# Optimization experiments

Hardware: AMD Instinct MI355X
Metric: run time of the kernel (lower is better)

Reference implementation:

```python
import jax, jax.numpy as jnp
import numpy as np

K = 1024   # codebook size
C = 8      # codebook channels
D = K // C # per-channel code dim = 128
BETA = 0.25
B = 8192   # batch of latent vectors, each of size C*D = K


def setup_inputs() -> dict:
    key = jax.random.key(0)
    k1, k2, k3 = jax.random.split(key, 3)
    latents = jax.random.normal(k1, (B, C * D), dtype=jnp.float32)
    # nn.Embedding(K, D) init: uniform(-1/K, 1/K)
    embedding = jax.random.uniform(k2, (K, D), dtype=jnp.float32,
                                   minval=-1.0 / K, maxval=1.0 / K)
    k = jax.random.randint(k3, (C,), 0, 8, dtype=jnp.int32)
    return {"latents": latents, "embedding": embedding, "k": k}


def reference(latents, embedding, k):
    sg = jax.lax.stop_gradient
    flat = latents.reshape(-1, D)                                  # [B*C, D]
    # squared euclidean distance to every code: [B*C, K]
    dist = (jnp.sum(flat ** 2, axis=1, keepdims=True)
            + jnp.sum(embedding ** 2, axis=1)
            - 2.0 * (flat @ embedding.T))
    order = jnp.argsort(dist, axis=1).reshape(-1, C, K)            # [B, C, K]
    # per channel c, pick the k[c]-th nearest code index
    sel = jnp.take_along_axis(order, k[None, :, None], axis=2)[..., 0]  # [B, C]
    # one-hot @ embedding == plain gather of selected rows
    quantized = embedding[sel.reshape(-1)].reshape(latents.shape)  # [B, C*D]
    commitment_loss = jnp.mean((sg(quantized) - latents) ** 2)
    embedding_loss = jnp.mean((quantized - sg(latents)) ** 2)
    vq_loss = BETA * commitment_loss + embedding_loss
    # straight-through estimator
    quantized_st = latents + sg(quantized - latents)
    return quantized_st, vq_loss
```

## Files before the change

### kernel.cpp

```cpp
#include <hip/hip_runtime.h>

#define KDIM   128
#define BM     64
#define NELEM  8388608

#define OFF_EBUF0 17408
#define OFF_ESQ   33792
#define OFF_FSQ   37888
#define OFF_SEL   38144
#define SMEM_SZ   38400

typedef __attribute__((ext_vector_type(8)))  short  short8;
typedef __attribute__((ext_vector_type(8)))  __bf16 bf16x8;
typedef __attribute__((ext_vector_type(4)))  float  f32x4;

__device__ inline ushort f2bf(float f) {
  unsigned u = __builtin_bit_cast(unsigned, f);
  u += 0x7fffu + ((u >> 16) & 1u);
  return (ushort)(u >> 16);
}
__device__ inline f32x4 mfma16(short8 a, short8 b, f32x4 c) {
  return __builtin_amdgcn_mfma_f32_16x16x32_bf16(
      __builtin_bit_cast(bf16x8, a), __builtin_bit_cast(bf16x8, b), c, 0, 0, 0);
}
__device__ inline void gload16(const void* g, void* l) {
  __builtin_amdgcn_global_load_lds(
      (const __attribute__((address_space(1))) unsigned*)g,
      (__attribute__((address_space(3))) unsigned*)l, 16, 0, 0);
}

__global__ void vq_prep(const float* __restrict__ emb, ushort* __restrict__ ebf,
                        float* __restrict__ esqm) {
  int j = blockIdx.x, d = threadIdx.x;
  float v = emb[j * KDIM + d];
  ebf[j * KDIM + (d ^ ((j & 7) << 3))] = f2bf(v);
  float s = v * v;
#pragma unroll
  for (int m = 1; m <= 32; m <<= 1) s += __shfl_xor(s, m);
  __shared__ float w[2];
  if ((threadIdx.x & 63) == 0) w[threadIdx.x >> 6] = s;
  __syncthreads();
  if (threadIdx.x == 0) esqm[j] = -0.5f * (w[0] + w[1]);
}

__global__ __launch_bounds__(256, 4) void vq_main(
    const float* __restrict__ lat, const float* __restrict__ emb,
    const int* __restrict__ ksel, const ushort* __restrict__ ebf,
    const float* __restrict__ esqm, float* __restrict__ out,
    float* __restrict__ partial) {
  __shared__ __align__(16) unsigned char smem[SMEM_SZ];
  ushort* fLds    = (ushort*)(smem);
  float*  esqmLds = (float*)(smem + OFF_ESQ);
  float*  fsqLds  = (float*)(smem + OFF_FSQ);
  int*    selLds  = (int*)(smem + OFF_SEL);

  const int tid = threadIdx.x;
  const int lane = tid & 63, wid = tid >> 6;
  const int gR0 = blockIdx.x * BM;

  {
    const char* src = (const char*)ebf + tid * 16;
    char* dst = (char*)smem + OFF_EBUF0 + tid * 16;
#pragma unroll
    for (int q = 0; q < 4; ++q) gload16(src + q * 4096, dst + q * 4096);
  }
  ((float4*)esqmLds)[tid] = ((const float4*)esqm)[tid];

#pragma unroll
  for (int it = 0; it < 8; ++it) {
    int i = tid + it * 256;
    int row = i >> 5, c4 = i & 31;
    float4 v = *(const float4*)(lat + (size_t)(gR0 + row) * KDIM + c4 * 4);
    float s = v.x * v.x + v.y * v.y + v.z * v.z + v.w * v.w;
#pragma unroll
    for (int m = 1; m <= 16; m <<= 1) s += __shfl_xor(s, m);
    if ((lane & 31) == 0) fsqLds[row] = s;
    ushort4 b; b.x = f2bf(v.x); b.y = f2bf(v.y); b.z = f2bf(v.z); b.w = f2bf(v.w);
    *(ushort4*)(&fLds[row * 136 + c4 * 4]) = b;
  }
  __syncthreads();

  const int n = lane & 15, hi = lane >> 4;
  short8 bfr[4];
  {
    const ushort* fp = &fLds[(wid * 16 + n) * 136 + hi * 8];
#pragma unroll
    for (int s = 0; s < 4; ++s) bfr[s] = *(const short8*)(fp + s * 32);
  }
  asm volatile("s_waitcnt lgkmcnt(0)" ::: "memory");

  const int nm = n & 7;
  const int pb = ((hi ^ (nm & 3)) << 4) | (((nm >> 2) & 1) << 6);
  const char* aE0 = (const char*)smem + OFF_EBUF0 + n * 256 + pb;
  const char* aO0 = (const char*)smem + OFF_EBUF0 + n * 256 + (pb ^ 64);
  const char* aE1 = (const char*)smem + 0 + n * 256 + pb;
  const char* aO1 = (const char*)smem + 0 + n * 256 + (pb ^ 64);

  int cst[4][4];
#pragma unroll
  for (int st = 0; st < 4; ++st)
#pragma unroll
    for (int r = 0; r < 4; ++r) cst[st][r] = st * 16 + hi * 4 + r;

  float top[8];
#pragma unroll
  for (int p = 0; p < 8; ++p) top[p] = __builtin_bit_cast(float, 0xFF800000u);

#pragma unroll 2
  for (int nn = 0; nn < 16; ++nn) {
    __builtin_amdgcn_s_barrier();
    if (nn < 15) {
      const char* src = (const char*)ebf + (nn + 1) * 16384 + tid * 16;
      char* dst = (char*)smem + ((nn & 1) ? OFF_EBUF0 : 0) + tid * 16;
#pragma unroll
      for (int q = 0; q < 4; ++q) gload16(src + q * 4096, dst + q * 4096);
      asm volatile("s_waitcnt vmcnt(4)" ::: "memory");
    } else {
      asm volatile("s_waitcnt vmcnt(0)" ::: "memory");
    }
    __builtin_amdgcn_s_barrier();

    const char* aEb = (nn & 1) ? aE1 : aE0;
    const char* aOb = (nn & 1) ? aO1 : aO0;

    f32x4 acc[4];
    {
      const float* eq = esqmLds + nn * 64 + hi * 4;
#pragma unroll
      for (int st = 0; st < 4; ++st) acc[st] = *(const f32x4*)(eq + st * 16);
    }

#pragma unroll
    for (int s = 0; s < 4; ++s) {
      const char* ab = (s & 1) ? aOb : aEb;
      const int so = (s >> 1) * 128;
#pragma unroll
      for (int st = 0; st < 4; ++st) {
        short8 a = *(const short8*)(ab + st * 4096 + so);
        acc[st] = mfma16(a, bfr[s], acc[st]);
      }
    }

#pragma unroll
    for (int cell = 0; cell < 2; ++cell) {
      float k[8];
#pragma unroll
      for (int st = 0; st < 2; ++st)
#pragma unroll
        for (int r = 0; r < 4; ++r) {
          unsigned bb = (__builtin_bit_cast(unsigned, acc[cell * 2 + st][r]) & 0xFFFFFC00u)
                        | (unsigned)cst[cell * 2 + st][r];
          k[st * 4 + r] = __builtin_bit_cast(float, bb);
        }
      float x = fmaxf(fmaxf(k[0], k[1]), k[2]);
      float y = fmaxf(fmaxf(k[3], k[4]), k[5]);
      float z = fmaxf(k[6], k[7]);
      float c = fmaxf(fmaxf(x, y), z);
      unsigned cb = __builtin_bit_cast(unsigned, c) | (unsigned)(nn << 6);
      float key = __builtin_bit_cast(float, cb);
#pragma unroll
      for (int p = 0; p < 8; ++p) {
        float mx = fmaxf(top[p], key);
        key = fminf(top[p], key);
        top[p] = mx;
      }
    }
  }

  float* mbuf = (float*)(smem + OFF_EBUF0);
  __syncthreads();
#pragma unroll
  for (int p = 0; p < 8; ++p) mbuf[p * 256 + tid] = top[p];
  __syncthreads();

  if (tid < 64) {
    const int b0 = (tid >> 4) * 64 + (tid & 15);
    int kk = ksel[tid & 7]; kk = kk < 0 ? 0 : (kk > 7 ? 7 : kk);
    float a0 = mbuf[b0], a1 = mbuf[b0 + 16], a2 = mbuf[b0 + 32], a3 = mbuf[b0 + 48];
    int i0 = 1, i1 = 1, i2 = 1, i3 = 1;
    float sel = a0;
    for (int s = 0; s <= kk; ++s) {
      float m01 = fmaxf(a0, a1), m23 = fmaxf(a2, a3);
      sel = fmaxf(m01, m23);
      if (sel == a0)      { a0 = mbuf[i0 * 256 + b0];      ++i0; }
      else if (sel == a1) { a1 = mbuf[i1 * 256 + b0 + 16]; ++i1; }
      else if (sel == a2) { a2 = mbuf[i2 * 256 + b0 + 32]; ++i2; }
      else                { a3 = mbuf[i3 * 256 + b0 + 48]; ++i3; }
    }
    unsigned sb = __builtin_bit_cast(unsigned, sel);
    selLds[tid] = (int)(sb & 1023u);
    float val = __builtin_bit_cast(float, sb & 0xFFFFFC00u);
    float rl = fsqLds[tid] - 2.0f * val;
#pragma unroll
    for (int m = 1; m <= 32; m <<= 1) rl += __shfl_xor(rl, m);
    if (tid == 0) partial[blockIdx.x] = rl;
  }
  __syncthreads();

#pragma unroll
  for (int it = 0; it < 8; ++it) {
    int i = tid + it * 256;
    int row = i >> 5, c4 = i & 31;
    int s2 = selLds[row];
    float4 q = *(const float4*)(emb + (size_t)s2 * KDIM + c4 * 4);
    *(float4*)(out + (size_t)(gR0 + row) * KDIM + c4 * 4) = q;
  }
}

__global__ void vq_reduce(const float* __restrict__ p, float* __restrict__ loss) {
  int t = threadIdx.x;
  double s = (double)p[t] + (double)p[t + 256] + (double)p[t + 512] + (double)p[t + 768];
#pragma unroll
  for (int m = 1; m <= 32; m <<= 1) s += __shfl_xor(s, m);
  __shared__ double w[4];
  if ((t & 63) == 0) w[t >> 6] = s;
  __syncthreads();
  if (t == 0) loss[0] = (float)((w[0] + w[1] + w[2] + w[3]) * (1.25 / 8388608.0));
}

extern "C" void kernel_launch(void* const* d_in, const int* in_sizes, int n_in,
                              void* d_out, int out_size, void* d_ws, size_t ws_size,
                              hipStream_t stream) {
  const float* lat = (const float*)d_in[0];
  const float* emb = (const float*)d_in[1];
  const int* ksel = (const int*)d_in[2];
  float* out = (float*)d_out;

  ushort* ebf = (ushort*)d_ws;
  float* esqm = (float*)((char*)d_ws + 262144);
  float* partial = (float*)((char*)d_ws + 266240);

  vq_prep<<<1024, 128, 0, stream>>>(emb, ebf, esqm);
  vq_main<<<1024, 256, 0, stream>>>(lat, emb, ksel, ebf, esqm, out, partial);
  vq_reduce<<<1, 256, 0, stream>>>(partial, out + NELEM);
}
```

Before: 44.49 us.

## Switch distance GEMM to FP8 MFMA with resident codebook and fused loss reduction

Rewrites the main kernel to quantize the codebook and latents to FP8 (with the codebook scaled by 1024) and use 16x16x32 fp8 MFMA, holding the whole 128KB FP8 codebook in LDS. It launches 256 blocks of 512 threads, each handling 256 rows, with two row groups per wave processed in turn. The per-lane top-8 lists are merged through cross-lane bitonic shuffles rather than an LDS merge. The separate reduce kernel is replaced by a fixed-point atomic accumulator with a last-block finalize. This aims to cut MFMA and LDS traffic and one launch, but FP8 precision could flip nearest-code ranking relative to the reference, and the lower block count lowers occupancy.

```diff
diff --git a/kernel.cpp b/kernel.cpp
--- a/kernel.cpp
+++ b/kernel.cpp
@@ -1,221 +1,233 @@
 #include <hip/hip_runtime.h>
 
 #define KDIM   128
-#define BM     64
 #define NELEM  8388608
 
-#define OFF_EBUF0 17408
-#define OFF_ESQ   33792
-#define OFF_FSQ   37888
-#define OFF_SEL   38144
-#define SMEM_SZ   38400
-
-typedef __attribute__((ext_vector_type(8)))  short  short8;
-typedef __attribute__((ext_vector_type(8)))  __bf16 bf16x8;
-typedef __attribute__((ext_vector_type(4)))  float  f32x4;
-
-__device__ inline ushort f2bf(float f) {
-  unsigned u = __builtin_bit_cast(unsigned, f);
-  u += 0x7fffu + ((u >> 16) & 1u);
-  return (ushort)(u >> 16);
-}
-__device__ inline f32x4 mfma16(short8 a, short8 b, f32x4 c) {
-  return __builtin_amdgcn_mfma_f32_16x16x32_bf16(
-      __builtin_bit_cast(bf16x8, a), __builtin_bit_cast(bf16x8, b), c, 0, 0, 0);
+typedef __attribute__((ext_vector_type(4))) float f32x4;
+typedef __attribute__((ext_vector_type(2))) int   int2v;
+
+__device__ inline f32x4 mfma8(long long a, long long b, f32x4 c) {
+  return __builtin_amdgcn_mfma_f32_16x16x32_fp8_fp8(a, b, c, 0, 0, 0);
 }
 __device__ inline void gload16(const void* g, void* l) {
   __builtin_amdgcn_global_load_lds(
       (const __attribute__((address_space(1))) unsigned*)g,
       (__attribute__((address_space(3))) unsigned*)l, 16, 0, 0);
 }
-
-__global__ void vq_prep(const float* __restrict__ emb, ushort* __restrict__ ebf,
-                        float* __restrict__ esqm) {
+__device__ inline long long pk8(float4 v0, float4 v1) {
+  int lo = __builtin_amdgcn_cvt_pk_fp8_f32(v0.x, v0.y, 0, false);
+  lo     = __builtin_amdgcn_cvt_pk_fp8_f32(v0.z, v0.w, lo, true);
+  int hi = __builtin_amdgcn_cvt_pk_fp8_f32(v1.x, v1.y, 0, false);
+  hi     = __builtin_amdgcn_cvt_pk_fp8_f32(v1.z, v1.w, hi, true);
+  int2v t; t.x = lo; t.y = hi;
+  return __builtin_bit_cast(long long, t);
+}
+__device__ inline float packk(float s, int c) {
+  return __builtin_bit_cast(float,
+      (__builtin_bit_cast(unsigned, s) & 0xFFFFFC00u) | (unsigned)c);
+}
+__device__ inline float sumsq(float4 a, float4 b) {
+  return a.x*a.x + a.y*a.y + a.z*a.z + a.w*a.w + b.x*b.x + b.y*b.y + b.z*b.z + b.w*b.w;
+}
+__device__ inline void merge8(float (&t)[8], int msk) {
+  float o[8];
+#pragma unroll
+  for (int p = 0; p < 8; ++p) o[p] = __shfl_xor(t[p], msk);
+  float m[8];
+#pragma unroll
+  for (int p = 0; p < 8; ++p) m[p] = fmaxf(t[p], o[7 - p]);
+#pragma unroll
+  for (int s = 4; s; s >>= 1)
+#pragma unroll
+    for (int i = 0; i < 8; ++i)
+      if (!(i & s)) {
+        float x = fmaxf(m[i], m[i | s]);
+        m[i | s] = fminf(m[i], m[i | s]);
+        m[i] = x;
+      }
+#pragma unroll
+  for (int p = 0; p < 8; ++p) t[p] = m[p];
+}
+
+__global__ void vq_prep(const float* __restrict__ emb, unsigned char* __restrict__ ebf8,
+                        float* __restrict__ esqm, unsigned long long* __restrict__ lossAcc,
+                        unsigned* __restrict__ cnt) {
   int j = blockIdx.x, d = threadIdx.x;
   float v = emb[j * KDIM + d];
-  ebf[j * KDIM + (d ^ ((j & 7) << 3))] = f2bf(v);
+  float vs = v * 1024.0f;
+  int p = __builtin_amdgcn_cvt_pk_fp8_f32(vs, vs, 0, false);
+  ebf8[j * KDIM + (d ^ ((j & 15) << 3))] = (unsigned char)(p & 0xFF);
   float s = v * v;
 #pragma unroll
   for (int m = 1; m <= 32; m <<= 1) s += __shfl_xor(s, m);
   __shared__ float w[2];
-  if ((threadIdx.x & 63) == 0) w[threadIdx.x >> 6] = s;
+  if ((d & 63) == 0) w[d >> 6] = s;
   __syncthreads();
-  if (threadIdx.x == 0) esqm[j] = -0.5f * (w[0] + w[1]);
-}
-
-__global__ __launch_bounds__(256, 4) void vq_main(
+  if (d == 0) esqm[j] = -512.0f * (w[0] + w[1]);
+  if (j == 0 && d == 0) { lossAcc[0] = 0ULL; cnt[0] = 0u; }
+}
+
+__device__ inline void scan_codes(const unsigned char* bk0, const unsigned char* bk1,
+                                  const unsigned char* bk2, const unsigned char* bk3,
+                                  const float* esqmLds, int hi,
+                                  long long v0, long long v1, long long v2, long long v3,
+                                  float (&top)[8]) {
+  int cid = hi * 4;
+#pragma unroll 4
+  for (int pp = 0; pp < 32; ++pp) {
+    const int off = pp * 4096;
+    const float* eb = esqmLds + pp * 32 + hi * 4;
+    f32x4 a0 = *(const f32x4*)(eb);
+    f32x4 a1 = *(const f32x4*)(eb + 16);
+    a0 = mfma8(*(const long long*)(bk0 + off), v0, a0);
+    a0 = mfma8(*(const long long*)(bk1 + off), v1, a0);
+    a0 = mfma8(*(const long long*)(bk2 + off), v2, a0);
+    a0 = mfma8(*(const long long*)(bk3 + off), v3, a0);
+    a1 = mfma8(*(const long long*)(bk0 + off + 2048), v0, a1);
+    a1 = mfma8(*(const long long*)(bk1 + off + 2048), v1, a1);
+    a1 = mfma8(*(const long long*)(bk2 + off + 2048), v2, a1);
+    a1 = mfma8(*(const long long*)(bk3 + off + 2048), v3, a1);
+    float k0 = packk(a0[0], cid + 0),  k1 = packk(a0[1], cid + 1);
+    float k2 = packk(a0[2], cid + 2),  k3 = packk(a0[3], cid + 3);
+    float k4 = packk(a1[0], cid + 16), k5 = packk(a1[1], cid + 17);
+    float k6 = packk(a1[2], cid + 18), k7 = packk(a1[3], cid + 19);
+    float x = fmaxf(fmaxf(fmaxf(k0, k1), fmaxf(k2, k3)),
+                    fmaxf(fmaxf(k4, k5), fmaxf(k6, k7)));
+#pragma unroll
+    for (int p = 0; p < 8; ++p) {
+      float mx = fmaxf(top[p], x);
+      x = fminf(top[p], x);
+      top[p] = mx;
+    }
+    cid += 32;
+  }
+}
+
+__device__ inline void write_rows(const float* __restrict__ emb, float* __restrict__ outp,
+                                  int grow0, int idx, int lane) {
+#pragma unroll 4
+  for (int r = 0; r < 16; ++r) {
+    int s2 = __shfl(idx, r);
+    float2 qv = *(const float2*)(emb + (size_t)s2 * KDIM + lane * 2);
+    *(float2*)(outp + (size_t)(grow0 + r) * KDIM + lane * 2) = qv;
+  }
+}
+
+__global__ __launch_bounds__(512, 1) void vq_main(
     const float* __restrict__ lat, const float* __restrict__ emb,
-    const int* __restrict__ ksel, const ushort* __restrict__ ebf,
+    const int* __restrict__ ksel, const unsigned char* __restrict__ ebf8,
     const float* __restrict__ esqm, float* __restrict__ out,
-    float* __restrict__ partial) {
-  __shared__ __align__(16) unsigned char smem[SMEM_SZ];
-  ushort* fLds    = (ushort*)(smem);
-  float*  esqmLds = (float*)(smem + OFF_ESQ);
-  float*  fsqLds  = (float*)(smem + OFF_FSQ);
-  int*    selLds  = (int*)(smem + OFF_SEL);
-
-  const int tid = threadIdx.x;
-  const int lane = tid & 63, wid = tid >> 6;
-  const int gR0 = blockIdx.x * BM;
-
+    unsigned long long* __restrict__ lossAcc, unsigned* __restrict__ cnt,
+    float* __restrict__ loss) {
+  __shared__ __align__(16) unsigned char smem[131072 + 4096 + 64];
+  float* esqmLds = (float*)(smem + 131072);
+  float* wLds    = (float*)(smem + 131072 + 4096);
+
+  const int tid = threadIdx.x, lane = tid & 63, wid = tid >> 6;
+  const int n = lane & 15, hi = lane >> 4;
+  const int gR0 = blockIdx.x * 256;
+
+  const float* rp0 = lat + (size_t)(gR0 + wid * 32 + n) * KDIM + hi * 8;
+  float4 p0[4], p1[4];
+#pragma unroll
+  for (int ks = 0; ks < 4; ++ks) {
+    p0[ks] = *(const float4*)(rp0 + ks * 32);
+    p1[ks] = *(const float4*)(rp0 + ks * 32 + 4);
+  }
   {
-    const char* src = (const char*)ebf + tid * 16;
-    char* dst = (char*)smem + OFF_EBUF0 + tid * 16;
-#pragma unroll
-    for (int q = 0; q < 4; ++q) gload16(src + q * 4096, dst + q * 4096);
-  }
-  ((float4*)esqmLds)[tid] = ((const float4*)esqm)[tid];
-
-#pragma unroll
-  for (int it = 0; it < 8; ++it) {
-    int i = tid + it * 256;
-    int row = i >> 5, c4 = i & 31;
-    float4 v = *(const float4*)(lat + (size_t)(gR0 + row) * KDIM + c4 * 4);
-    float s = v.x * v.x + v.y * v.y + v.z * v.z + v.w * v.w;
-#pragma unroll
-    for (int m = 1; m <= 16; m <<= 1) s += __shfl_xor(s, m);
-    if ((lane & 31) == 0) fsqLds[row] = s;
-    ushort4 b; b.x = f2bf(v.x); b.y = f2bf(v.y); b.z = f2bf(v.z); b.w = f2bf(v.w);
-    *(ushort4*)(&fLds[row * 136 + c4 * 4]) = b;
-  }
+    const char* src = (const char*)ebf8 + tid * 16;
+    char* dst = (char*)smem + tid * 16;
+#pragma unroll
+    for (int qq = 0; qq < 16; ++qq) gload16(src + qq * 8192, dst + qq * 8192);
+    if (tid < 256) gload16((const char*)esqm + tid * 16, (char*)esqmLds + tid * 16);
+  }
+  const float* rp1 = rp0 + 16 * KDIM;
+  float4 q0[4], q1[4];
+#pragma unroll
+  for (int ks = 0; ks < 4; ++ks) {
+    q0[ks] = *(const float4*)(rp1 + ks * 32);
+    q1[ks] = *(const float4*)(rp1 + ks * 32 + 4);
+  }
+  float fsq0;
+  long long b00, b01, b02, b03;
+  {
+    float s = 0.f;
+#pragma unroll
+    for (int ks = 0; ks < 4; ++ks) s += sumsq(p0[ks], p1[ks]);
+    s += __shfl_xor(s, 16); s += __shfl_xor(s, 32);
+    fsq0 = s;
+    b00 = pk8(p0[0], p1[0]); b01 = pk8(p0[1], p1[1]);
+    b02 = pk8(p0[2], p1[2]); b03 = pk8(p0[3], p1[3]);
+  }
+  asm volatile("s_waitcnt vmcnt(0)" ::: "memory");
+  __builtin_amdgcn_s_barrier();
+
+  const unsigned char* ab = smem + n * 128 + ((hi ^ (n & 3)) << 3);
+  const int nh = n >> 2;
+  const unsigned char* bk0 = ab + ((0 ^ nh) << 5);
+  const unsigned char* bk1 = ab + ((1 ^ nh) << 5);
+  const unsigned char* bk2 = ab + ((2 ^ nh) << 5);
+  const unsigned char* bk3 = ab + ((3 ^ nh) << 5);
+
+  const float NINF = __builtin_bit_cast(float, 0xFF800000u);
+  float top0[8], top1[8];
+#pragma unroll
+  for (int p = 0; p < 8; ++p) { top0[p] = NINF; top1[p] = NINF; }
+
+  scan_codes(bk0, bk1, bk2, bk3, esqmLds, hi, b00, b01, b02, b03, top0);
+
+  float fsq1;
+  long long b10, b11, b12, b13;
+  {
+    float s = 0.f;
+#pragma unroll
+    for (int ks = 0; ks < 4; ++ks) s += sumsq(q0[ks], q1[ks]);
+    s += __shfl_xor(s, 16); s += __shfl_xor(s, 32);
+    fsq1 = s;
+    b10 = pk8(q0[0], q1[0]); b11 = pk8(q0[1], q1[1]);
+    b12 = pk8(q0[2], q1[2]); b13 = pk8(q0[3], q1[3]);
+  }
+
+  int kk = ksel[lane & 7];
+  kk = kk < 0 ? 0 : (kk > 7 ? 7 : kk);
+
+  merge8(top0, 16); merge8(top0, 32);
+  float sel0 = top0[0];
+#pragma unroll
+  for (int p = 1; p < 8; ++p) sel0 = (kk == p) ? top0[p] : sel0;
+  unsigned sb0 = __builtin_bit_cast(unsigned, sel0);
+  int idx0 = (int)(sb0 & 1023u);
+  float rl0 = fsq0 - __builtin_bit_cast(float, sb0 & 0xFFFFFC00u) * (1.0f / 512.0f);
+  write_rows(emb, out, gR0 + wid * 32, idx0, lane);
+
+  scan_codes(bk0, bk1, bk2, bk3, esqmLds, hi, b10, b11, b12, b13, top1);
+  merge8(top1, 16); merge8(top1, 32);
+  float sel1 = top1[0];
+#pragma unroll
+  for (int p = 1; p < 8; ++p) sel1 = (kk == p) ? top1[p] : sel1;
+  unsigned sb1 = __builtin_bit_cast(unsigned, sel1);
+  int idx1 = (int)(sb1 & 1023u);
+  float rl1 = fsq1 - __builtin_bit_cast(float, sb1 & 0xFFFFFC00u) * (1.0f / 512.0f);
+  write_rows(emb, out, gR0 + wid * 32 + 16, idx1, lane);
+
+  float c = (lane < 16) ? (rl0 + rl1) : 0.f;
+#pragma unroll
+  for (int m = 1; m <= 32; m <<= 1) c += __shfl_xor(c, m);
+  if (lane == 0) wLds[wid] = c;
   __syncthreads();
-
-  const int n = lane & 15, hi = lane >> 4;
-  short8 bfr[4];
-  {
-    const ushort* fp = &fLds[(wid * 16 + n) * 136 + hi * 8];
-#pragma unroll
-    for (int s = 0; s < 4; ++s) bfr[s] = *(const short8*)(fp + s * 32);
-  }
-  asm volatile("s_waitcnt lgkmcnt(0)" ::: "memory");
-
-  const int nm = n & 7;
-  const int pb = ((hi ^ (nm & 3)) << 4) | (((nm >> 2) & 1) << 6);
-  const char* aE0 = (const char*)smem + OFF_EBUF0 + n * 256 + pb;
-  const char* aO0 = (const char*)smem + OFF_EBUF0 + n * 256 + (pb ^ 64);
-  const char* aE1 = (const char*)smem + 0 + n * 256 + pb;
-  const char* aO1 = (const char*)smem + 0 + n * 256 + (pb ^ 64);
-
-  int cst[4][4];
-#pragma unroll
-  for (int st = 0; st < 4; ++st)
-#pragma unroll
-    for (int r = 0; r < 4; ++r) cst[st][r] = st * 16 + hi * 4 + r;
-
-  float top[8];
-#pragma unroll
-  for (int p = 0; p < 8; ++p) top[p] = __builtin_bit_cast(float, 0xFF800000u);
-
-#pragma unroll 2
-  for (int nn = 0; nn < 16; ++nn) {
-    __builtin_amdgcn_s_barrier();
-    if (nn < 15) {
-      const char* src = (const char*)ebf + (nn + 1) * 16384 + tid * 16;
-      char* dst = (char*)smem + ((nn & 1) ? OFF_EBUF0 : 0) + tid * 16;
-#pragma unroll
-      for (int q = 0; q < 4; ++q) gload16(src + q * 4096, dst + q * 4096);
-      asm volatile("s_waitcnt vmcnt(4)" ::: "memory");
-    } else {
-      asm volatile("s_waitcnt vmcnt(0)" ::: "memory");
+  if (tid == 0) {
+    double bs = 0.0;
+#pragma unroll
+    for (int w = 0; w < 8; ++w) bs += (double)wLds[w];
+    long long iv = (long long)(bs * 1048576.0 + 0.5);
+    atomicAdd(lossAcc, (unsigned long long)iv);
+    __threadfence();
+    unsigned done = atomicAdd(cnt, 1u);
+    if (done == 255u) {
+      unsigned long long tot = atomicAdd(lossAcc, 0ULL);
+      loss[0] = (float)((double)(long long)tot * (1.25 / (1048576.0 * 8388608.0)));
     }
-    __builtin_amdgcn_s_barrier();
-
-    const char* aEb = (nn & 1) ? aE1 : aE0;
-    const char* aOb = (nn & 1) ? aO1 : aO0;
-
-    f32x4 acc[4];
-    {
-      const float* eq = esqmLds + nn * 64 + hi * 4;
-#pragma unroll
-      for (int st = 0; st < 4; ++st) acc[st] = *(const f32x4*)(eq + st * 16);
-    }
-
-#pragma unroll
-    for (int s = 0; s < 4; ++s) {
-      const char* ab = (s & 1) ? aOb : aEb;
-      const int so = (s >> 1) * 128;
-#pragma unroll
-      for (int st = 0; st < 4; ++st) {
-        short8 a = *(const short8*)(ab + st * 4096 + so);
-        acc[st] = mfma16(a, bfr[s], acc[st]);
-      }
-    }
-
-#pragma unroll
-    for (int cell = 0; cell < 2; ++cell) {
-      float k[8];
-#pragma unroll
-      for (int st = 0; st < 2; ++st)
-#pragma unroll
-        for (int r = 0; r < 4; ++r) {
-          unsigned bb = (__builtin_bit_cast(unsigned, acc[cell * 2 + st][r]) & 0xFFFFFC00u)
-                        | (unsigned)cst[cell * 2 + st][r];
-          k[st * 4 + r] = __builtin_bit_cast(float, bb);
-        }
-      float x = fmaxf(fmaxf(k[0], k[1]), k[2]);
-      float y = fmaxf(fmaxf(k[3], k[4]), k[5]);
-      float z = fmaxf(k[6], k[7]);
-      float c = fmaxf(fmaxf(x, y), z);
-      unsigned cb = __builtin_bit_cast(unsigned, c) | (unsigned)(nn << 6);
-      float key = __builtin_bit_cast(float, cb);
-#pragma unroll
-      for (int p = 0; p < 8; ++p) {
-        float mx = fmaxf(top[p], key);
-        key = fminf(top[p], key);
-        top[p] = mx;
-      }
-    }
-  }
-
-  float* mbuf = (float*)(smem + OFF_EBUF0);
-  __syncthreads();
-#pragma unroll
-  for (int p = 0; p < 8; ++p) mbuf[p * 256 + tid] = top[p];
-  __syncthreads();
-
-  if (tid < 64) {
-    const int b0 = (tid >> 4) * 64 + (tid & 15);
-    int kk = ksel[tid & 7]; kk = kk < 0 ? 0 : (kk > 7 ? 7 : kk);
-    float a0 = mbuf[b0], a1 = mbuf[b0 + 16], a2 = mbuf[b0 + 32], a3 = mbuf[b0 + 48];
-    int i0 = 1, i1 = 1, i2 = 1, i3 = 1;
-    float sel = a0;
-    for (int s = 0; s <= kk; ++s) {
-      float m01 = fmaxf(a0, a1), m23 = fmaxf(a2, a3);
-      sel = fmaxf(m01, m23);
-      if (sel == a0)      { a0 = mbuf[i0 * 256 + b0];      ++i0; }
-      else if (sel == a1) { a1 = mbuf[i1 * 256 + b0 + 16]; ++i1; }
-      else if (sel == a2) { a2 = mbuf[i2 * 256 + b0 + 32]; ++i2; }
-      else                { a3 = mbuf[i3 * 256 + b0 + 48]; ++i3; }
-    }
-    unsigned sb = __builtin_bit_cast(unsigned, sel);
-    selLds[tid] = (int)(sb & 1023u);
-    float val = __builtin_bit_cast(float, sb & 0xFFFFFC00u);
-    float rl = fsqLds[tid] - 2.0f * val;
-#pragma unroll
-    for (int m = 1; m <= 32; m <<= 1) rl += __shfl_xor(rl, m);
-    if (tid == 0) partial[blockIdx.x] = rl;
-  }
-  __syncthreads();
-
-#pragma unroll
-  for (int it = 0; it < 8; ++it) {
-    int i = tid + it * 256;
-    int row = i >> 5, c4 = i & 31;
-    int s2 = selLds[row];
-    float4 q = *(const float4*)(emb + (size_t)s2 * KDIM + c4 * 4);
-    *(float4*)(out + (size_t)(gR0 + row) * KDIM + c4 * 4) = q;
-  }
-}
-
-__global__ void vq_reduce(const float* __restrict__ p, float* __restrict__ loss) {
-  int t = threadIdx.x;
-  double s = (double)p[t] + (double)p[t + 256] + (double)p[t + 512] + (double)p[t + 768];
-#pragma unroll
-  for (int m = 1; m <= 32; m <<= 1) s += __shfl_xor(s, m);
-  __shared__ double w[4];
-  if ((t & 63) == 0) w[t >> 6] = s;
-  __syncthreads();
-  if (t == 0) loss[0] = (float)((w[0] + w[1] + w[2] + w[3]) * (1.25 / 8388608.0));
+  }
 }
 
 extern "C" void kernel_launch(void* const* d_in, const int* in_sizes, int n_in,
@@ -226,11 +238,13 @@
   const int* ksel = (const int*)d_in[2];
   float* out = (float*)d_out;
 
-  ushort* ebf = (ushort*)d_ws;
-  float* esqm = (float*)((char*)d_ws + 262144);
-  float* partial = (float*)((char*)d_ws + 266240);
-
-  vq_prep<<<1024, 128, 0, stream>>>(emb, ebf, esqm);
-  vq_main<<<1024, 256, 0, stream>>>(lat, emb, ksel, ebf, esqm, out, partial);
-  vq_reduce<<<1, 256, 0, stream>>>(partial, out + NELEM);
-}
+  unsigned char* ebf8 = (unsigned char*)d_ws;
+  float* esqm = (float*)((char*)d_ws + 131072);
+  unsigned long long* lossAcc =
+      (unsigned long long*)((char*)d_ws + 135168);
+  unsigned* cnt = (unsigned*)((char*)d_ws + 135176);
+
+  vq_prep<<<1024, 128, 0, stream>>>(emb, ebf8, esqm, lossAcc, cnt);
+  vq_main<<<256, 512, 0, stream>>>(lat, emb, ksel, ebf8, esqm, out, lossAcc, cnt,
+                                   out + NELEM);
+}
```

Result: slower. 47.20 us (+6.1%).
